# Performance work log

Hardware: AMD Instinct MI355X
Metric: run time of the kernel (lower is better)

Reference implementation:

```python
import jax, jax.numpy as jnp
import numpy as np

N_EMBEDDING = 32
HEAD_SIZE = 64
B, T = 8, 4096


def setup_inputs() -> dict:
    key = jax.random.key(0)
    kx, kk, kq, kv = jax.random.split(key, 4)
    x = jax.random.normal(kx, (B, T, N_EMBEDDING), dtype=jnp.float32)
    Wk = jax.random.normal(kk, (N_EMBEDDING, HEAD_SIZE), dtype=jnp.float32) * 0.05
    Wq = jax.random.normal(kq, (N_EMBEDDING, HEAD_SIZE), dtype=jnp.float32) * 0.05
    Wv = jax.random.normal(kv, (N_EMBEDDING, HEAD_SIZE), dtype=jnp.float32) * 0.05
    return {"x": x, "Wk": Wk, "Wq": Wq, "Wv": Wv}


def reference(x, Wk, Wq, Wv):
    # x: [B, T, C]; projections (no bias)
    k = jnp.einsum("btc,cd->btd", x, Wk)  # [B,T,D]
    q = jnp.einsum("btc,cd->btd", x, Wq)
    v = jnp.einsum("btc,cd->btd", x, Wv)
    # raw scores (NOTE: original module applies no 1/sqrt(D) scaling)
    wei = jnp.einsum("bqd,bkd->bqk", q, k)  # [B,T,T]
    t = x.shape[1]
    causal = jnp.tril(jnp.ones((t, t), dtype=bool))
    wei = jnp.where(causal[None, :, :], wei, -jnp.inf)
    wei = jax.nn.softmax(wei, axis=-1)
    out = jnp.einsum("bqk,bkd->bqd", wei, v)  # [B,T,D]
    return out
```

## Files before the change

kernel.cpp:

```cpp
#include <hip/hip_runtime.h>
#include <hip/hip_bf16.h>

constexpr int Bc = 8;
constexpr int Tt = 4096;
constexpr int Dd = 64;

typedef __attribute__((ext_vector_type(8))) short short8;
typedef __attribute__((ext_vector_type(4))) float floatx4;
typedef uint4   __attribute__((may_alias)) uint4_a;
typedef short8  __attribute__((may_alias)) short8_a;
typedef ushort4 __attribute__((may_alias)) ushort4_a;
typedef float4  __attribute__((may_alias)) float4_a;

#define MFMA16(A, B, C) __builtin_amdgcn_mfma_f32_16x16x32_bf16(A, B, C, 0, 0, 0)
constexpr float LOG2E = 1.4426950408889634f;

__device__ __forceinline__ unsigned rnd16(float x) {
    unsigned u; __builtin_memcpy(&u, &x, 4); return u + 0x8000u;
}
__device__ __forceinline__ unsigned pk_bf2(float lo, float hi) {
    return __builtin_amdgcn_perm(rnd16(hi), rnd16(lo), 0x07060302);
}
__device__ __forceinline__ ushort4 pack4(floatx4 d) {
    union { unsigned u[2]; ushort4 v; } r;
    r.u[0] = pk_bf2(d[0], d[1]);
    r.u[1] = pk_bf2(d[2], d[3]);
    return r.v;
}
__device__ __forceinline__ short8 cvt8(float4 a, float4 b) {
    union { unsigned u[4]; short8 s; } r;
    r.u[0] = pk_bf2(a.x, a.y);
    r.u[1] = pk_bf2(a.z, a.w);
    r.u[2] = pk_bf2(b.x, b.y);
    r.u[3] = pk_bf2(b.z, b.w);
    return r.s;
}

__global__ __launch_bounds__(1024) void attn_kernel(
    const float* __restrict__ x,
    const float* __restrict__ Wk, const float* __restrict__ Wq,
    const float* __restrict__ Wv,
    float* __restrict__ out)
{
    __shared__ uint4 sStage[4096];
    __shared__ uint4 sP[2048];

    int b  = blockIdx.x & 7;
    int pr = blockIdx.x >> 3;
    int tid  = threadIdx.x;
    int wave = tid >> 6, lane = tid & 63;
    int group = wave >> 2, gw = wave & 3;
    int ln15 = lane & 15, quad = lane >> 4;
    size_t bT = (size_t)b * Tt;

    short8 wk_f[4], wv_f[4];
    #pragma unroll
    for (int c = 0; c < 4; ++c) {
        int col = 16*c + ln15;
        union { unsigned u[4]; short8 s; } rk, rv;
        #pragma unroll
        for (int jj = 0; jj < 4; ++jj) {
            const float* k0 = Wk + (quad*8 + 2*jj) * 64 + col;
            const float* v0 = Wv + (quad*8 + 2*jj) * 64 + col;
            rk.u[jj] = pk_bf2(k0[0], k0[64]);
            rv.u[jj] = pk_bf2(v0[0], v0[64]);
        }
        wk_f[c] = rk.s; wv_f[c] = rv.s;
    }
    short8 wq_f;
    {
        int dt = wave >> 2, colD = 16*dt + ln15;
        union { unsigned u[4]; short8 s; } rq;
        #pragma unroll
        for (int jj = 0; jj < 4; ++jj) {
            const float* qp = Wq + (quad*8 + 2*jj) * 64 + colD;
            rq.u[jj] = pk_bf2(qp[0] * LOG2E, qp[64] * LOG2E);
        }
        wq_f = rq.s;
    }

    const int stK = group * 1024;
    const int stV = group * 1024 + 512;
    unsigned short* sSh = (unsigned short*)sStage;
    const int stK_h = stK * 8, stV_h = stV * 8;

    #pragma unroll
    for (int phase = 0; phase < 2; ++phase) {
        const int qtP = (phase == 0) ? (63 - pr) : pr;
        const int q0 = qtP * 64;
        const int qrow = q0 + gw*16 + ln15;

        {
            int qs = wave & 3, dt = wave >> 2;
            const float* xp = x + (bT + q0 + qs*16 + ln15)*32 + quad*8;
            float4 x0 = ((const float4_a*)xp)[0];
            float4 x1 = ((const float4_a*)xp)[1];
            short8 xq = cvt8(x0, x1);
            floatx4 d = (floatx4){0.f, 0.f, 0.f, 0.f};
            d = MFMA16(wq_f, xq, d);
            int ql = qs*16 + ln15;
            int graw = 2*dt + (quad >> 1);
            unsigned short* sQh = (unsigned short*)sP;
            *(ushort4_a*)(sQh + ql*64 + ((graw ^ (ql & 7)) << 3)
                              + ((quad & 1) << 2)) = pack4(d);
        }
        __syncthreads();
        short8 bq0, bq1;
        {
            int ql = gw*16 + ln15;
            union { uint4 u; short8 s; } t0, t1;
            t0.u = sP[ql*8 + (quad ^ (ql & 7))];
            t1.u = sP[ql*8 + ((quad + 4) ^ (ql & 7))];
            bq0 = t0.s; bq1 = t1.s;
        }
        floatx4 o4[4];
        #pragma unroll
        for (int c = 0; c < 4; ++c) o4[c] = (floatx4){0.f, 0.f, 0.f, 0.f};
        float l_lane = 0.f;

        const int nIter = (qtP + 4) >> 2;
        float4 pX0, pX1;
        if (group <= qtP) {
            const float* xp = x + (bT + group*64 + 16*gw + ln15)*32 + quad*8;
            pX0 = ((const float4_a*)xp)[0];
            pX1 = ((const float4_a*)xp)[1];
        }

        for (int it = 0; it < nIter; ++it) {
            int kt = 4*it + group;
            bool active = (kt <= qtP);
            __syncthreads();
            if (active) {
                short8 xf = cvt8(pX0, pX1);
                int key = 16*gw + ln15;
                #pragma unroll
                for (int c = 0; c < 4; ++c) {
                    floatx4 dk = (floatx4){0.f, 0.f, 0.f, 0.f};
                    dk = MFMA16(wk_f[c], xf, dk);
                    int g1 = 2*c + (quad >> 1);
                    *(ushort4_a*)(sSh + stK_h + key*64 + ((g1 ^ (key & 7)) << 3)
                                      + ((quad & 1) << 2)) = pack4(dk);
                    floatx4 dv = (floatx4){0.f, 0.f, 0.f, 0.f};
                    dv = MFMA16(xf, wv_f[c], dv);
                    int dcol = 16*c + ln15;
                    int g2 = 2*gw + (quad >> 1);
                    *(ushort4_a*)(sSh + stV_h + dcol*64 + ((g2 ^ (dcol & 7)) << 3)
                                      + ((quad & 1) << 2)) = pack4(dv);
                }
            }
            int ktn = kt + 4;
            if (ktn <= qtP) {
                const float* xp = x + (bT + ktn*64 + 16*gw + ln15)*32 + quad*8;
                pX0 = ((const float4_a*)xp)[0];
                pX1 = ((const float4_a*)xp)[1];
            }
            __syncthreads();
            if (!active) continue;
            int k0 = kt * 64;

            floatx4 s4[4];
            #pragma unroll
            for (int t = 0; t < 4; ++t) {
                int kr = 16*t + ln15;
                union { uint4 u; short8 s; } a0, a1;
                a0.u = sStage[stK + kr*8 + (quad ^ (ln15 & 7))];
                a1.u = sStage[stK + kr*8 + ((quad + 4) ^ (ln15 & 7))];
                floatx4 c = (floatx4){0.f, 0.f, 0.f, 0.f};
                c = MFMA16(a0.s, bq0, c);
                c = MFMA16(a1.s, bq1, c);
                s4[t] = c;
            }

            unsigned long long* sP64 = (unsigned long long*)sP;
            const int pb = wave*256 + ln15*16;
            const int xk = ln15 & 14;
            if (kt == qtP) {
                #pragma unroll
                for (int t = 0; t < 4; ++t) {
                    int keyb = k0 + 16*t + quad*4;
                    float p[4];
                    #pragma unroll
                    for (int r = 0; r < 4; ++r) {
                        p[r] = (keyb + r <= qrow) ? __builtin_amdgcn_exp2f(s4[t][r]) : 0.f;
                        l_lane += p[r];
                    }
                    unsigned long long pk =
                        ((unsigned long long)pk_bf2(p[2], p[3]) << 32) | pk_bf2(p[0], p[1]);
                    sP64[pb + ((4*t + quad) ^ xk)] = pk;
                }
            } else {
                #pragma unroll
                for (int t = 0; t < 4; ++t) {
                    float p[4];
                    #pragma unroll
                    for (int r = 0; r < 4; ++r) {
                        p[r] = __builtin_amdgcn_exp2f(s4[t][r]);
                        l_lane += p[r];
                    }
                    unsigned long long pk =
                        ((unsigned long long)pk_bf2(p[2], p[3]) << 32) | pk_bf2(p[0], p[1]);
                    sP64[pb + ((4*t + quad) ^ xk)] = pk;
                }
            }

            int h = (ln15 >> 1) & 7;
            union { uint4 u; short8 s; } p0, p1;
            p0.u = sP[wave*128 + ln15*8 + (quad ^ h)];
            p1.u = sP[wave*128 + ln15*8 + ((quad + 4) ^ h)];
            #pragma unroll
            for (int c = 0; c < 4; ++c) {
                int dr = 16*c + ln15;
                union { uint4 u; short8 s; } v0, v1;
                v0.u = sStage[stV + dr*8 + (quad ^ (dr & 7))];
                v1.u = sStage[stV + dr*8 + ((quad + 4) ^ (dr & 7))];
                o4[c] = MFMA16(v0.s, p0.s, o4[c]);
                o4[c] = MFMA16(v1.s, p1.s, o4[c]);
            }
        }

        __syncthreads();
        int li = gw*64 + lane;
        ((float*)sP)[wave*64 + lane] = l_lane;
        if (group != 0) {
            float4* st = (float4*)(sStage + group*1024);
            #pragma unroll
            for (int c = 0; c < 4; ++c)
                st[c*256 + li] = make_float4(o4[c][0], o4[c][1], o4[c][2], o4[c][3]);
        }
        __syncthreads();
        if (group == 0) {
            float l = l_lane + ((float*)sP)[256 + li]
                    + ((float*)sP)[512 + li] + ((float*)sP)[768 + li];
            l += __shfl_xor(l, 16);
            l += __shfl_xor(l, 32);
            float inv = 1.f / l;
            #pragma unroll
            for (int c = 0; c < 4; ++c) {
                float ax = o4[c][0], ay = o4[c][1], az = o4[c][2], aw = o4[c][3];
                #pragma unroll
                for (int g = 1; g < 4; ++g) {
                    float4 p = ((float4*)(sStage + g*1024))[c*256 + li];
                    ax += p.x; ay += p.y; az += p.z; aw += p.w;
                }
                *(float4_a*)(out + (bT + q0 + gw*16 + ln15) * Dd + 16*c + quad*4)
                    = make_float4(ax*inv, ay*inv, az*inv, aw*inv);
            }
        }
        __syncthreads();
    }
}

extern "C" void kernel_launch(void* const* d_in, const int* in_sizes, int n_in,
                              void* d_out, int out_size, void* d_ws, size_t ws_size,
                              hipStream_t stream)
{
    const float* x  = (const float*)d_in[0];
    const float* Wk = (const float*)d_in[1];
    const float* Wq = (const float*)d_in[2];
    const float* Wv = (const float*)d_in[3];
    float* out = (float*)d_out;

    attn_kernel<<<Bc * 32, 1024, 0, stream>>>(x, Wk, Wq, Wv, out);
}
```

Baseline: 102.9 us.

## Fold Wq·Wkᵀ into a 32x32 matrix and apply Wv after attention

Precomputes G = Wq·Wkᵀ (32x32, log2e-scaled) once per block, so scores become (xG)·x over 32 channels instead of q·k over 64. The PV product now runs against raw x, and Wv is applied once per query row at the end. This removes the per-tile K/V projection MFMAs, halves the shared staging buffer, and halves the score and PV MFMA counts. In exchange it adds extra bf16 rounding of G and of the intermediate z, a transposed x staging path using strided scalar global loads, and an epilogue MFMA.

```diff
diff --git a/kernel.cpp b/kernel.cpp
--- a/kernel.cpp
+++ b/kernel.cpp
@@ -42,7 +42,7 @@
     const float* __restrict__ Wv,
     float* __restrict__ out)
 {
-    __shared__ uint4 sStage[4096];
+    __shared__ uint4 sStage[2048];
     __shared__ uint4 sP[2048];
 
     int b  = blockIdx.x & 7;
@@ -51,79 +51,105 @@
     int wave = tid >> 6, lane = tid & 63;
     int group = wave >> 2, gw = wave & 3;
     int ln15 = lane & 15, quad = lane >> 4;
+    int tid_g = tid & 255;
     size_t bT = (size_t)b * Tt;
 
-    short8 wk_f[4], wv_f[4];
+    short8 wv_f[4];
     #pragma unroll
-    for (int c = 0; c < 4; ++c) {
-        int col = 16*c + ln15;
-        union { unsigned u[4]; short8 s; } rk, rv;
+    for (int t = 0; t < 4; ++t) {
+        int col = 16*t + ln15;
+        union { unsigned u[4]; short8 s; } rv;
         #pragma unroll
         for (int jj = 0; jj < 4; ++jj) {
-            const float* k0 = Wk + (quad*8 + 2*jj) * 64 + col;
             const float* v0 = Wv + (quad*8 + 2*jj) * 64 + col;
-            rk.u[jj] = pk_bf2(k0[0], k0[64]);
             rv.u[jj] = pk_bf2(v0[0], v0[64]);
         }
-        wk_f[c] = rk.s; wv_f[c] = rv.s;
-    }
-    short8 wq_f;
-    {
-        int dt = wave >> 2, colD = 16*dt + ln15;
-        union { unsigned u[4]; short8 s; } rq;
-        #pragma unroll
-        for (int jj = 0; jj < 4; ++jj) {
-            const float* qp = Wq + (quad*8 + 2*jj) * 64 + colD;
-            rq.u[jj] = pk_bf2(qp[0] * LOG2E, qp[64] * LOG2E);
-        }
-        wq_f = rq.s;
-    }
-
-    const int stK = group * 1024;
-    const int stV = group * 1024 + 512;
-    unsigned short* sSh = (unsigned short*)sStage;
-    const int stK_h = stK * 8, stV_h = stV * 8;
+        wv_f[t] = rv.s;
+    }
+
+    if (wave == 0) {
+        floatx4 gC[2][2];
+        #pragma unroll
+        for (int mt = 0; mt < 2; ++mt)
+            #pragma unroll
+            for (int nt = 0; nt < 2; ++nt) gC[mt][nt] = (floatx4){0.f,0.f,0.f,0.f};
+        #pragma unroll
+        for (int kt = 0; kt < 2; ++kt) {
+            short8 aG[2], bG[2];
+            #pragma unroll
+            for (int mt = 0; mt < 2; ++mt) {
+                const float* qp = Wq + (ln15 + 16*mt)*64 + 32*kt + quad*8;
+                float4 a = ((const float4_a*)qp)[0], bb = ((const float4_a*)qp)[1];
+                a.x*=LOG2E; a.y*=LOG2E; a.z*=LOG2E; a.w*=LOG2E;
+                bb.x*=LOG2E; bb.y*=LOG2E; bb.z*=LOG2E; bb.w*=LOG2E;
+                aG[mt] = cvt8(a, bb);
+                const float* kp = Wk + (ln15 + 16*mt)*64 + 32*kt + quad*8;
+                bG[mt] = cvt8(((const float4_a*)kp)[0], ((const float4_a*)kp)[1]);
+            }
+            #pragma unroll
+            for (int mt = 0; mt < 2; ++mt)
+                #pragma unroll
+                for (int nt = 0; nt < 2; ++nt)
+                    gC[mt][nt] = MFMA16(aG[mt], bG[nt], gC[mt][nt]);
+        }
+        unsigned short* sGh = (unsigned short*)sP;
+        #pragma unroll
+        for (int mt = 0; mt < 2; ++mt)
+            #pragma unroll
+            for (int nt = 0; nt < 2; ++nt)
+                *(ushort4_a*)(sGh + (16*nt + ln15)*32 + 16*mt + quad*4)
+                    = pack4(gC[mt][nt]);
+    }
+    __syncthreads();
+    short8 gt[2];
+    #pragma unroll
+    for (int mt = 0; mt < 2; ++mt) {
+        union { uint4 u; short8 s; } g;
+        g.u = sP[(16*mt + ln15)*4 + quad];
+        gt[mt] = g.s;
+    }
+    __syncthreads();
+
+    const int stB = group * 512;
+    const int cT = tid_g & 31, kgT = tid_g >> 5;
+    unsigned short* sYh = (unsigned short*)sP;
 
     #pragma unroll
     for (int phase = 0; phase < 2; ++phase) {
-        const int qtP = (phase == 0) ? (63 - pr) : pr;
+        const int qtP = phase ? pr : 63 - pr;
         const int q0 = qtP * 64;
         const int qrow = q0 + gw*16 + ln15;
 
+        if (wave < 8) {
+            int qs = wave & 3, mt = wave >> 2;
+            const float* xp = x + (bT + q0 + qs*16 + ln15)*32 + quad*8;
+            short8 xq = cvt8(((const float4_a*)xp)[0], ((const float4_a*)xp)[1]);
+            floatx4 d = (floatx4){0.f,0.f,0.f,0.f};
+            d = MFMA16(gt[mt], xq, d);
+            *(ushort4_a*)(sYh + (qs*16 + ln15)*32 + 16*mt + quad*4) = pack4(d);
+        }
+        __syncthreads();
+        short8 bq;
         {
-            int qs = wave & 3, dt = wave >> 2;
-            const float* xp = x + (bT + q0 + qs*16 + ln15)*32 + quad*8;
-            float4 x0 = ((const float4_a*)xp)[0];
-            float4 x1 = ((const float4_a*)xp)[1];
-            short8 xq = cvt8(x0, x1);
-            floatx4 d = (floatx4){0.f, 0.f, 0.f, 0.f};
-            d = MFMA16(wq_f, xq, d);
-            int ql = qs*16 + ln15;
-            int graw = 2*dt + (quad >> 1);
-            unsigned short* sQh = (unsigned short*)sP;
-            *(ushort4_a*)(sQh + ql*64 + ((graw ^ (ql & 7)) << 3)
-                              + ((quad & 1) << 2)) = pack4(d);
-        }
-        __syncthreads();
-        short8 bq0, bq1;
-        {
-            int ql = gw*16 + ln15;
-            union { uint4 u; short8 s; } t0, t1;
-            t0.u = sP[ql*8 + (quad ^ (ql & 7))];
-            t1.u = sP[ql*8 + ((quad + 4) ^ (ql & 7))];
-            bq0 = t0.s; bq1 = t1.s;
-        }
-        floatx4 o4[4];
-        #pragma unroll
-        for (int c = 0; c < 4; ++c) o4[c] = (floatx4){0.f, 0.f, 0.f, 0.f};
+            union { uint4 u; short8 s; } t0;
+            t0.u = sP[(gw*16 + ln15)*4 + quad];
+            bq = t0.s;
+        }
+
+        floatx4 z4[2];
+        z4[0] = (floatx4){0.f,0.f,0.f,0.f};
+        z4[1] = (floatx4){0.f,0.f,0.f,0.f};
         float l_lane = 0.f;
 
         const int nIter = (qtP + 4) >> 2;
-        float4 pX0, pX1;
+        float4 pX0, pX1; float pT[8];
         if (group <= qtP) {
             const float* xp = x + (bT + group*64 + 16*gw + ln15)*32 + quad*8;
             pX0 = ((const float4_a*)xp)[0];
             pX1 = ((const float4_a*)xp)[1];
+            const float* tp = x + (bT + group*64 + kgT*8)*32 + cT;
+            #pragma unroll
+            for (int j = 0; j < 8; ++j) pT[j] = tp[j*32];
         }
 
         for (int it = 0; it < nIter; ++it) {
@@ -131,28 +157,22 @@
             bool active = (kt <= qtP);
             __syncthreads();
             if (active) {
-                short8 xf = cvt8(pX0, pX1);
-                int key = 16*gw + ln15;
-                #pragma unroll
-                for (int c = 0; c < 4; ++c) {
-                    floatx4 dk = (floatx4){0.f, 0.f, 0.f, 0.f};
-                    dk = MFMA16(wk_f[c], xf, dk);
-                    int g1 = 2*c + (quad >> 1);
-                    *(ushort4_a*)(sSh + stK_h + key*64 + ((g1 ^ (key & 7)) << 3)
-                                      + ((quad & 1) << 2)) = pack4(dk);
-                    floatx4 dv = (floatx4){0.f, 0.f, 0.f, 0.f};
-                    dv = MFMA16(xf, wv_f[c], dv);
-                    int dcol = 16*c + ln15;
-                    int g2 = 2*gw + (quad >> 1);
-                    *(ushort4_a*)(sSh + stV_h + dcol*64 + ((g2 ^ (dcol & 7)) << 3)
-                                      + ((quad & 1) << 2)) = pack4(dv);
-                }
+                union { short8 s; uint4 u; } xu;
+                xu.s = cvt8(pX0, pX1);
+                sStage[stB + (16*gw + ln15)*4 + quad] = xu.u;
+                uint4 xt;
+                xt.x = pk_bf2(pT[0], pT[1]); xt.y = pk_bf2(pT[2], pT[3]);
+                xt.z = pk_bf2(pT[4], pT[5]); xt.w = pk_bf2(pT[6], pT[7]);
+                sStage[stB + 256 + cT*8 + (kgT ^ (cT & 7))] = xt;
             }
             int ktn = kt + 4;
             if (ktn <= qtP) {
                 const float* xp = x + (bT + ktn*64 + 16*gw + ln15)*32 + quad*8;
                 pX0 = ((const float4_a*)xp)[0];
                 pX1 = ((const float4_a*)xp)[1];
+                const float* tp = x + (bT + ktn*64 + kgT*8)*32 + cT;
+                #pragma unroll
+                for (int j = 0; j < 8; ++j) pT[j] = tp[j*32];
             }
             __syncthreads();
             if (!active) continue;
@@ -161,13 +181,10 @@
             floatx4 s4[4];
             #pragma unroll
             for (int t = 0; t < 4; ++t) {
-                int kr = 16*t + ln15;
-                union { uint4 u; short8 s; } a0, a1;
-                a0.u = sStage[stK + kr*8 + (quad ^ (ln15 & 7))];
-                a1.u = sStage[stK + kr*8 + ((quad + 4) ^ (ln15 & 7))];
-                floatx4 c = (floatx4){0.f, 0.f, 0.f, 0.f};
-                c = MFMA16(a0.s, bq0, c);
-                c = MFMA16(a1.s, bq1, c);
+                union { uint4 u; short8 s; } a;
+                a.u = sStage[stB + (16*t + ln15)*4 + quad];
+                floatx4 c = (floatx4){0.f,0.f,0.f,0.f};
+                c = MFMA16(a.s, bq, c);
                 s4[t] = c;
             }
 
@@ -208,13 +225,13 @@
             p0.u = sP[wave*128 + ln15*8 + (quad ^ h)];
             p1.u = sP[wave*128 + ln15*8 + ((quad + 4) ^ h)];
             #pragma unroll
-            for (int c = 0; c < 4; ++c) {
-                int dr = 16*c + ln15;
-                union { uint4 u; short8 s; } v0, v1;
-                v0.u = sStage[stV + dr*8 + (quad ^ (dr & 7))];
-                v1.u = sStage[stV + dr*8 + ((quad + 4) ^ (dr & 7))];
-                o4[c] = MFMA16(v0.s, p0.s, o4[c]);
-                o4[c] = MFMA16(v1.s, p1.s, o4[c]);
+            for (int mt = 0; mt < 2; ++mt) {
+                int row = 16*mt + ln15;
+                union { uint4 u; short8 s; } a0, a1;
+                a0.u = sStage[stB + 256 + row*8 + (quad ^ (ln15 & 7))];
+                a1.u = sStage[stB + 256 + row*8 + ((4 + quad) ^ (ln15 & 7))];
+                z4[mt] = MFMA16(a0.s, p0.s, z4[mt]);
+                z4[mt] = MFMA16(a1.s, p1.s, z4[mt]);
             }
         }
 
@@ -222,10 +239,9 @@
         int li = gw*64 + lane;
         ((float*)sP)[wave*64 + lane] = l_lane;
         if (group != 0) {
-            float4* st = (float4*)(sStage + group*1024);
-            #pragma unroll
-            for (int c = 0; c < 4; ++c)
-                st[c*256 + li] = make_float4(o4[c][0], o4[c][1], o4[c][2], o4[c][3]);
+            float4* st = (float4*)((char*)sStage + group*8192);
+            st[li*2 + 0] = make_float4(z4[0][0], z4[0][1], z4[0][2], z4[0][3]);
+            st[li*2 + 1] = make_float4(z4[1][0], z4[1][1], z4[1][2], z4[1][3]);
         }
         __syncthreads();
         if (group == 0) {
@@ -235,15 +251,24 @@
             l += __shfl_xor(l, 32);
             float inv = 1.f / l;
             #pragma unroll
-            for (int c = 0; c < 4; ++c) {
-                float ax = o4[c][0], ay = o4[c][1], az = o4[c][2], aw = o4[c][3];
-                #pragma unroll
-                for (int g = 1; g < 4; ++g) {
-                    float4 p = ((float4*)(sStage + g*1024))[c*256 + li];
-                    ax += p.x; ay += p.y; az += p.z; aw += p.w;
-                }
-                *(float4_a*)(out + (bT + q0 + gw*16 + ln15) * Dd + 16*c + quad*4)
-                    = make_float4(ax*inv, ay*inv, az*inv, aw*inv);
+            for (int g = 1; g < 4; ++g) {
+                float4* st = (float4*)((char*)sStage + g*8192);
+                float4 a = st[li*2 + 0], bb = st[li*2 + 1];
+                z4[0][0]+=a.x; z4[0][1]+=a.y; z4[0][2]+=a.z; z4[0][3]+=a.w;
+                z4[1][0]+=bb.x; z4[1][1]+=bb.y; z4[1][2]+=bb.z; z4[1][3]+=bb.w;
+            }
+            unsigned short* sZb = (unsigned short*)sStage;
+            #pragma unroll
+            for (int mt = 0; mt < 2; ++mt)
+                *(ushort4_a*)(sZb + (gw*16 + ln15)*32 + 16*mt + quad*4) = pack4(z4[mt]);
+            union { uint4 u; short8 s; } zb;
+            zb.u = sStage[(gw*16 + ln15)*4 + quad];
+            #pragma unroll
+            for (int t = 0; t < 4; ++t) {
+                floatx4 o = (floatx4){0.f,0.f,0.f,0.f};
+                o = MFMA16(wv_f[t], zb.s, o);
+                *(float4_a*)(out + (bT + q0 + gw*16 + ln15)*Dd + 16*t + quad*4)
+                    = make_float4(o[0]*inv, o[1]*inv, o[2]*inv, o[3]*inv);
             }
         }
         __syncthreads();
```

Result: slower. 108.8 us (+5.7%).
